# Optimization experiments

Hardware: AMD Instinct MI355X
Metric: run time of the kernel (lower is better)

## Reference

```python
import jax, jax.numpy as jnp
import numpy as np
from jax import lax

K_TOP = 4
NF1, NF2 = 6, 14
KS1, KS2 = 7, 5


def conv1d_grouped(x, w, b, groups, pad):
    # x: (B, Cin, L), w: (Cout, Cin//groups, K)
    y = lax.conv_general_dilated(x, w, window_strides=(1,), padding=[(pad, pad)],
                                 dimension_numbers=('NCH', 'OIH', 'NCH'),
                                 feature_group_count=groups)
    return y + b[None, :, None]


def kmax_pool(x, k):
    # order-preserving k-max along last axis
    idx = jnp.sort(lax.top_k(x, k)[1], axis=-1)
    return jnp.take_along_axis(x, idx, axis=-1)


def fold_sum(h, b, nf, rows, L):
    # h: (B, rows*nf, L) with group-major channel layout (rows groups of nf)
    h = h.reshape(b, rows, nf, L).transpose(0, 2, 1, 3)        # (B, nf, rows, L)
    h = h.reshape(b, nf, rows // 2, 2, L).sum(axis=3)          # Fold(2,2): sum adjacent row pairs
    return h.transpose(0, 2, 1, 3).reshape(b, (rows // 2) * nf, L)


def setup_inputs() -> dict:
    key = jax.random.key(0)
    ks = jax.random.split(key, 8)
    V, D, C, B, S = 50257, 256, 1000, 32, 1024
    x = jax.random.randint(ks[0], (B, S), 0, V)
    emb = jax.random.normal(ks[1], (V, D), jnp.float32)
    w1 = jax.random.normal(ks[2], (NF1 * D, 1, KS1), jnp.float32) * 0.1
    b1 = jnp.zeros((NF1 * D,), jnp.float32)
    w2 = jax.random.normal(ks[3], (NF2 * (D // 2), NF1, KS2), jnp.float32) * 0.05
    b2 = jnp.zeros((NF2 * (D // 2),), jnp.float32)
    wf = jax.random.normal(ks[4], (C, NF2 * (D // 4) * K_TOP), jnp.float32) * 0.02
    bf = jnp.zeros((C,), jnp.float32)
    return {"x": x, "emb": emb, "w1": w1, "b1": b1, "w2": w2, "b2": b2, "wf": wf, "bf": bf}


def reference(x, emb, w1, b1, w2, b2, wf, bf):
    D = emb.shape[1]
    B = x.shape[0]
    h = emb[x].transpose(0, 2, 1)                 # (B, D, S)
    h = conv1d_grouped(h, w1, b1, groups=D, pad=KS1 - 1)   # (B, 6D, S+6)
    L1 = h.shape[-1]
    h = fold_sum(h, B, NF1, D, L1)                # (B, 3D, L1)
    # dynamic k-max: layer 1 of 2 -> k = max(k_top, ceil(L/2))
    k1 = max(K_TOP, -(-L1 // 2))
    h = jnp.tanh(kmax_pool(h, k1))
    h = conv1d_grouped(h, w2, b2, groups=D // 2, pad=KS2 - 1)  # (B, 7D, k1+4)
    L2 = h.shape[-1]
    h = fold_sum(h, B, NF2, D // 2, L2)           # (B, 14*(D/4), L2)
    h = jnp.tanh(kmax_pool(h, K_TOP))             # (B, 14*(D/4), k_top)
    # dropout is identity in eval mode
    h = h.reshape(B, -1)
    return h @ wf.T + bf
```

## Files before the change

### kernel.cpp

```cpp
#include <hip/hip_runtime.h>
#include <hip/hip_bf16.h>


typedef __attribute__((ext_vector_type(8))) short short8;
typedef __attribute__((ext_vector_type(4))) float f32x4;
typedef __attribute__((ext_vector_type(2))) float f32x2;
typedef __attribute__((ext_vector_type(4))) int int4v;

union VPack { int4v i; short8 s; };

__device__ __forceinline__ float fast_tanh(float x) {
    float e = __expf(2.f * x);
    return 1.f - 2.f / (e + 1.f);
}

__device__ __forceinline__ unsigned fkey(float f) {
    unsigned u = __float_as_uint(f);
    return (u & 0x80000000u) ? ~u : (u | 0x80000000u);
}

__device__ __forceinline__ float fkey_inv(unsigned k) {
    unsigned u = (k & 0x80000000u) ? (k ^ 0x80000000u) : ~k;
    return __uint_as_float(u);
}

__device__ __forceinline__ unsigned f2bf_rne(float f) {
    unsigned u = __float_as_uint(f);
    return (u + 0x7fffu + ((u >> 16) & 1u)) >> 16;
}

__device__ __forceinline__ int prefix_cnt(unsigned long long m) {
    return (int)__builtin_amdgcn_mbcnt_hi((unsigned)(m >> 32),
                 __builtin_amdgcn_mbcnt_lo((unsigned)m, 0u));
}

__global__ __launch_bounds__(896) void stage12_kernel(
    const int* __restrict__ x, const float* __restrict__ emb,
    const float* __restrict__ w1, const float* __restrict__ b1,
    const float* __restrict__ w2, const float* __restrict__ b2,
    __hip_bfloat16* __restrict__ H)
{
    __shared__ __align__(16) float X[7448];
    __shared__ __align__(16) unsigned F[12 * 536];
    const int hw = blockIdx.x;
    const int logical = ((hw & 7) << 8) | (hw >> 3);
    const int b = logical >> 6;
    const int r2 = logical & 63;
    const int tid = threadIdx.x;
    const int w = tid >> 6;
    const int lane = tid & 63;
    float* e = X;

    const int half = (w >= 6) ? 1 : 0;
    const int c0 = __builtin_amdgcn_readfirstlane(
        (2 * (2 * r2 + half)) * 6 + ((w < 12) ? (w - half * 6) : 0));
    const int c1 = c0 + 6;
    float wA[7], wB[7];
#pragma unroll
    for (int t = 0; t < 7; ++t) { wA[t] = w1[c0 * 7 + t]; wB[t] = w1[c1 * 7 + t]; }
    const float bias = b1[c0] + b1[c1];
    const int bidx2 = __builtin_amdgcn_readfirstlane((2 * r2) * 14 + w);
    const float bias2 = b2[bidx2] + b2[bidx2 + 14];

    {
        const int l0 = tid - 6;
        const int l1 = tid + 890;
        int t0 = -1, t1 = -1;
        if (l0 >= 0 && l0 < 1024) t0 = x[(b << 10) + l0];
        if (tid < 208 && l1 < 1024) t1 = x[(b << 10) + l1];
        float4 v0 = {0.f, 0.f, 0.f, 0.f}, v1 = {0.f, 0.f, 0.f, 0.f};
        if (t0 >= 0) v0 = *(const float4*)(emb + ((size_t)t0 << 8) + (r2 << 2));
        if (t1 >= 0) v1 = *(const float4*)(emb + ((size_t)t1 << 8) + (r2 << 2));
        for (int i = tid; i < 12 * 536; i += 896) F[i] = 0u;
        e[0 * 1104 + tid] = v0.x; e[1 * 1104 + tid] = v0.y;
        e[2 * 1104 + tid] = v0.z; e[3 * 1104 + tid] = v0.w;
        if (tid < 208) {
            const int idx = tid + 896;
            e[0 * 1104 + idx] = v1.x; e[1 * 1104 + idx] = v1.y;
            e[2 * 1104 + idx] = v1.z; e[3 * 1104 + idx] = v1.w;
        }
    }
    __syncthreads();

    if (w < 12) {
        const float* ep0 = e + (2 * half) * 1104;
        const float* ep1 = ep0 + 1104;
        f32x2 wv[7];
#pragma unroll
        for (int t = 0; t < 7; ++t) wv[t] = f32x2{wA[t], wB[t]};

        const int pos0 = lane * 17;
        f32x2 win[7];
#pragma unroll
        for (int t = 0; t < 7; ++t) win[t] = f32x2{ep0[pos0 + t], ep1[pos0 + t]};

        unsigned key[17];
#pragma unroll
        for (int j = 0; j < 17; ++j) {
            f32x2 acc = f32x2{bias, 0.f};
#pragma unroll
            for (int t = 0; t < 7; ++t) acc += win[t] * wv[t];
            float a = acc.x + acc.y;
            key[j] = (pos0 + j < 1030) ? fkey(a) : 0u;
            if (j < 16) {
#pragma unroll
                for (int t = 0; t < 6; ++t) win[t] = win[t + 1];
                win[6] = f32x2{ep0[pos0 + j + 7], ep1[pos0 + j + 7]};
            }
        }

        unsigned T = 0u;
        for (int bit = 31; bit >= 0; --bit) {
            unsigned cand = T | (1u << bit);
            int cnt = 0;
#pragma unroll
            for (int j = 0; j < 17; ++j) cnt += (int)__popcll(__ballot(key[j] >= cand));
            if (cnt >= 515) T = cand;
            if (cnt == 515) break;
        }

        int gt_tot = 0, gt_run = 0, eq_run = 0;
#pragma unroll
        for (int j = 0; j < 17; ++j) {
            unsigned long long bg = __ballot(key[j] > T);
            unsigned long long be = __ballot(key[j] == T);
            gt_tot += (int)__popcll(bg);
            gt_run += prefix_cnt(bg);
            eq_run += prefix_cnt(be);
        }
        const int q = 515 - gt_tot;
        unsigned* Frow = F + w * 536;
#pragma unroll
        for (int j = 0; j < 17; ++j) {
            bool isgt = key[j] > T;
            bool iseq = key[j] == T;
            int pos = gt_run + (eq_run < q ? eq_run : q);
            if (isgt || (iseq && eq_run < q)) Frow[4 + pos] = key[j];
            gt_run += isgt ? 1 : 0;
            eq_run += iseq ? 1 : 0;
        }

#pragma unroll
        for (int it = 0; it < 9; ++it) {
            int i = 4 + lane + (it << 6);
            if (i < 519) {
                unsigned k = Frow[i];
                float v = fast_tanh(fkey_inv(k));
                unsigned h = f2bf_rne(v);
                float fh = __uint_as_float(h << 16);
                unsigned l = f2bf_rne(v - fh);
                Frow[i] = (k == 0u) ? 0u : ((h << 16) | l);
            }
        }
    }

    const int jA = lane & 15;
    const int q3 = lane >> 4;
    short8 Ah0, Ah1, Al0, Al1;
    {
        float wt[16];
#pragma unroll
        for (int mm = 0; mm < 16; ++mm) {
            float v = 0.f;
            if (mm < 15 && jA < 14) {
                const int irow = 3 * q3 + mm / 5;
                const int t = mm % 5;
                const int h2 = (irow >= 6) ? 1 : 0;
                v = w2[(((2 * r2 + h2) * 14 + jA) * 6 + (irow - 6 * h2)) * 5 + t];
            }
            wt[mm] = v;
        }
#pragma unroll
        for (int m = 0; m < 8; ++m) {
            unsigned h0 = f2bf_rne(wt[m]);
            float fh0 = __uint_as_float(h0 << 16);
            Ah0[m] = (short)h0;
            Al0[m] = (short)f2bf_rne(wt[m] - fh0);
            unsigned h1 = f2bf_rne(wt[8 + m]);
            float fh1 = __uint_as_float(h1 << 16);
            Ah1[m] = (short)h1;
            Al1[m] = (short)f2bf_rne(wt[8 + m] - fh1);
        }
    }
    __syncthreads();

    float* OUT = X;
    for (int tile = w; tile < 33; tile += 14) {
        const int p0 = tile << 4;
        const int bidx = (3 * q3) * 536 + p0 + jA;
        unsigned u[16];
#pragma unroll
        for (int mm = 0; mm < 15; ++mm) u[mm] = F[bidx + (mm / 5) * 536 + (mm % 5)];
        u[15] = 0u;
        VPack bh0, bl0, bh1, bl1;
#pragma unroll
        for (int k = 0; k < 4; ++k) {
            unsigned a = u[2 * k], bq = u[2 * k + 1];
            bh0.i[k] = (int)((a >> 16) | (bq & 0xffff0000u));
            bl0.i[k] = (int)((a & 0xffffu) | (bq << 16));
            unsigned c = u[8 + 2 * k], d = u[9 + 2 * k];
            bh1.i[k] = (int)((c >> 16) | (d & 0xffff0000u));
            bl1.i[k] = (int)((c & 0xffffu) | (d << 16));
        }
        f32x4 d0 = {0.f, 0.f, 0.f, 0.f};
        f32x4 d1 = {0.f, 0.f, 0.f, 0.f};
        d0 = __builtin_amdgcn_mfma_f32_16x16x32_bf16(Ah0, bh0.s, d0, 0, 0, 0);
        d1 = __builtin_amdgcn_mfma_f32_16x16x32_bf16(Ah1, bh1.s, d1, 0, 0, 0);
        d0 = __builtin_amdgcn_mfma_f32_16x16x32_bf16(Ah0, bl0.s, d0, 0, 0, 0);
        d1 = __builtin_amdgcn_mfma_f32_16x16x32_bf16(Ah1, bl1.s, d1, 0, 0, 0);
        d0 = __builtin_amdgcn_mfma_f32_16x16x32_bf16(Al0, bh0.s, d0, 0, 0, 0);
        d1 = __builtin_amdgcn_mfma_f32_16x16x32_bf16(Al1, bh1.s, d1, 0, 0, 0);
        float* orow = OUT + (q3 * 4) * 532 + p0 + jA;
#pragma unroll
        for (int r = 0; r < 4; ++r)
            if (q3 * 4 + r < 14) orow[r * 532] = d0[r] + d1[r];
    }
    __syncthreads();

    {
        const int j = w;
        const int base = lane * 9;
        float vv[9];
#pragma unroll
        for (int jj = 0; jj < 9; ++jj)
            vv[jj] = (base + jj < 519) ? OUT[j * 532 + base + jj] : -INFINITY;
        float sv[4]; int si[4];
#pragma unroll
        for (int it = 0; it < 4; ++it) {
            float m = vv[0]; int mi = base;
#pragma unroll
            for (int jj = 1; jj < 9; ++jj) { if (vv[jj] > m) { m = vv[jj]; mi = base + jj; } }
#pragma unroll
            for (int d = 1; d < 64; d <<= 1) {
                float om = __shfl_xor(m, d, 64);
                int omi = __shfl_xor(mi, d, 64);
                if (om > m || (om == m && omi < mi)) { m = om; mi = omi; }
            }
            sv[it] = m; si[it] = mi;
            int lj = mi - base;
#pragma unroll
            for (int jj = 0; jj < 9; ++jj) if (jj == lj) vv[jj] = -INFINITY;
        }
#define CSWAP(a, bq) { if (si[a] > si[bq]) { int ti = si[a]; si[a] = si[bq]; si[bq] = ti; \
                                             float tv = sv[a]; sv[a] = sv[bq]; sv[bq] = tv; } }
        CSWAP(0, 1) CSWAP(2, 3) CSWAP(0, 2) CSWAP(1, 3) CSWAP(1, 2)
#undef CSWAP
        if (lane == 0) {
            __hip_bfloat16* op = H + (size_t)b * 3584 + (r2 * 14 + j) * 4;
#pragma unroll
            for (int k = 0; k < 4; ++k) op[k] = __float2bfloat16(fast_tanh(sv[k] + bias2));
        }
    }
}

__global__ __launch_bounds__(512) void stage3_kernel(
    const __hip_bfloat16* __restrict__ Hb, const float* __restrict__ wf,
    const float* __restrict__ bfv, float* __restrict__ out)
{
    __shared__ __align__(16) float sred[8 * 256];
    const int nt = blockIdx.x % 63;
    const int mh = blockIdx.x / 63;
    const int w = threadIdx.x >> 6, lane = threadIdx.x & 63;
    const int row = lane & 15, quad = lane >> 4;
    const int c = nt * 16 + row;
    const bool cvalid = (c < 1000);
    const int kofs = w * 448 + quad * 8;
    const __hip_bfloat16* ap = Hb + (size_t)(mh * 16 + row) * 3584 + kofs;
    const float* bp = wf + (size_t)(cvalid ? c : 0) * 3584 + kofs;

    f32x4 acc = {0.f, 0.f, 0.f, 0.f};
#pragma unroll
    for (int it = 0; it < 14; ++it) {
        short8 a0 = *(const short8*)(ap + it * 32);
        float4 p0 = *(const float4*)(bp + it * 32);
        float4 p1 = *(const float4*)(bp + it * 32 + 4);
        short8 bfr;
        bfr[0] = (short)f2bf_rne(p0.x); bfr[1] = (short)f2bf_rne(p0.y);
        bfr[2] = (short)f2bf_rne(p0.z); bfr[3] = (short)f2bf_rne(p0.w);
        bfr[4] = (short)f2bf_rne(p1.x); bfr[5] = (short)f2bf_rne(p1.y);
        bfr[6] = (short)f2bf_rne(p1.z); bfr[7] = (short)f2bf_rne(p1.w);
        if (!cvalid) bfr = short8{0, 0, 0, 0, 0, 0, 0, 0};
        acc = __builtin_amdgcn_mfma_f32_16x16x32_bf16(a0, bfr, acc, 0, 0, 0);
    }
#pragma unroll
    for (int r_ = 0; r_ < 4; ++r_) sred[w * 256 + lane * 4 + r_] = acc[r_];
    __syncthreads();
    if (threadIdx.x < 64) {
        const int l2 = threadIdx.x;
        const int rr = l2 & 15, qq = l2 >> 4;
        const int cc = nt * 16 + rr;
        if (cc < 1000) {
            const float bias = bfv[cc];
#pragma unroll
            for (int r_ = 0; r_ < 4; ++r_) {
                float s = 0.f;
#pragma unroll
                for (int ww = 0; ww < 8; ++ww) s += sred[ww * 256 + l2 * 4 + r_];
                int brow = mh * 16 + qq * 4 + r_;
                out[brow * 1000 + cc] = s + bias;
            }
        }
    }
}

extern "C" void kernel_launch(void* const* d_in, const int* in_sizes, int n_in,
                              void* d_out, int out_size, void* d_ws, size_t ws_size,
                              hipStream_t stream) {
    const int* x      = (const int*)d_in[0];
    const float* emb  = (const float*)d_in[1];
    const float* w1   = (const float*)d_in[2];
    const float* b1   = (const float*)d_in[3];
    const float* w2   = (const float*)d_in[4];
    const float* b2   = (const float*)d_in[5];
    const float* wf   = (const float*)d_in[6];
    const float* bfv  = (const float*)d_in[7];

    __hip_bfloat16* H = (__hip_bfloat16*)d_ws;

    stage12_kernel<<<32 * 64, 896, 0, stream>>>(x, emb, w1, b1, w2, b2, H);
    stage3_kernel<<<126, 512, 0, stream>>>(H, wf, bfv, (float*)d_out);
}
```

Before: 238.1 us.

## Split final GEMM over K with atomics and reuse weight tile across both batch halves

The final linear layer now splits the K dimension into 4 chunks across blocks. Each block processes both 16-row batch tiles, so every converted wf fragment is reused for two MFMAs instead of being loaded twice by separate blocks. Partial sums are combined with atomicAdd into an output that a new kernel pre-fills with the bias. This halves the wf traffic and bf16 conversions, at the cost of an extra launch and atomics. It also makes the fp32 summation order nondeterministic.

```diff
diff --git a/kernel.cpp b/kernel.cpp
--- a/kernel.cpp
+++ b/kernel.cpp
@@ -253,25 +253,35 @@
     }
 }
 
-__global__ __launch_bounds__(512) void stage3_kernel(
-    const __hip_bfloat16* __restrict__ Hb, const float* __restrict__ wf,
+__global__ __launch_bounds__(256) void bias_init_kernel(
     const float* __restrict__ bfv, float* __restrict__ out)
 {
-    __shared__ __align__(16) float sred[8 * 256];
+    int idx = blockIdx.x * 256 + threadIdx.x;
+    if (idx < 32000) out[idx] = bfv[idx - (idx / 1000) * 1000];
+}
+
+__global__ __launch_bounds__(256) void stage3_kernel(
+    const __hip_bfloat16* __restrict__ Hb, const float* __restrict__ wf,
+    float* __restrict__ out)
+{
+    __shared__ __align__(16) float sred[2 * 4 * 256];
     const int nt = blockIdx.x % 63;
-    const int mh = blockIdx.x / 63;
+    const int kc = blockIdx.x / 63;
     const int w = threadIdx.x >> 6, lane = threadIdx.x & 63;
     const int row = lane & 15, quad = lane >> 4;
     const int c = nt * 16 + row;
     const bool cvalid = (c < 1000);
-    const int kofs = w * 448 + quad * 8;
-    const __hip_bfloat16* ap = Hb + (size_t)(mh * 16 + row) * 3584 + kofs;
+    const int kofs = kc * 896 + w * 224 + quad * 8;
+    const __hip_bfloat16* ap0 = Hb + (size_t)row * 3584 + kofs;
+    const __hip_bfloat16* ap1 = ap0 + (size_t)16 * 3584;
     const float* bp = wf + (size_t)(cvalid ? c : 0) * 3584 + kofs;
 
-    f32x4 acc = {0.f, 0.f, 0.f, 0.f};
-#pragma unroll
-    for (int it = 0; it < 14; ++it) {
-        short8 a0 = *(const short8*)(ap + it * 32);
+    f32x4 acc0 = {0.f, 0.f, 0.f, 0.f};
+    f32x4 acc1 = {0.f, 0.f, 0.f, 0.f};
+#pragma unroll
+    for (int it = 0; it < 7; ++it) {
+        short8 a0 = *(const short8*)(ap0 + it * 32);
+        short8 a1 = *(const short8*)(ap1 + it * 32);
         float4 p0 = *(const float4*)(bp + it * 32);
         float4 p1 = *(const float4*)(bp + it * 32 + 4);
         short8 bfr;
@@ -280,24 +290,28 @@
         bfr[4] = (short)f2bf_rne(p1.x); bfr[5] = (short)f2bf_rne(p1.y);
         bfr[6] = (short)f2bf_rne(p1.z); bfr[7] = (short)f2bf_rne(p1.w);
         if (!cvalid) bfr = short8{0, 0, 0, 0, 0, 0, 0, 0};
-        acc = __builtin_amdgcn_mfma_f32_16x16x32_bf16(a0, bfr, acc, 0, 0, 0);
-    }
-#pragma unroll
-    for (int r_ = 0; r_ < 4; ++r_) sred[w * 256 + lane * 4 + r_] = acc[r_];
+        acc0 = __builtin_amdgcn_mfma_f32_16x16x32_bf16(a0, bfr, acc0, 0, 0, 0);
+        acc1 = __builtin_amdgcn_mfma_f32_16x16x32_bf16(a1, bfr, acc1, 0, 0, 0);
+    }
+#pragma unroll
+    for (int r_ = 0; r_ < 4; ++r_) {
+        sred[(0 * 4 + w) * 256 + lane * 4 + r_] = acc0[r_];
+        sred[(1 * 4 + w) * 256 + lane * 4 + r_] = acc1[r_];
+    }
     __syncthreads();
-    if (threadIdx.x < 64) {
-        const int l2 = threadIdx.x;
+    if (threadIdx.x < 128) {
+        const int mt = threadIdx.x >> 6;
+        const int l2 = threadIdx.x & 63;
         const int rr = l2 & 15, qq = l2 >> 4;
         const int cc = nt * 16 + rr;
         if (cc < 1000) {
-            const float bias = bfv[cc];
+            const float* sp = sred + mt * 4 * 256;
 #pragma unroll
             for (int r_ = 0; r_ < 4; ++r_) {
-                float s = 0.f;
-#pragma unroll
-                for (int ww = 0; ww < 8; ++ww) s += sred[ww * 256 + l2 * 4 + r_];
-                int brow = mh * 16 + qq * 4 + r_;
-                out[brow * 1000 + cc] = s + bias;
+                float s = sp[0 * 256 + l2 * 4 + r_] + sp[1 * 256 + l2 * 4 + r_]
+                        + sp[2 * 256 + l2 * 4 + r_] + sp[3 * 256 + l2 * 4 + r_];
+                int brow = mt * 16 + qq * 4 + r_;
+                atomicAdd(&out[brow * 1000 + cc], s);
             }
         }
     }
@@ -317,6 +331,7 @@
 
     __hip_bfloat16* H = (__hip_bfloat16*)d_ws;
 
+    bias_init_kernel<<<125, 256, 0, stream>>>(bfv, (float*)d_out);
     stage12_kernel<<<32 * 64, 896, 0, stream>>>(x, emb, w1, b1, w2, b2, H);
-    stage3_kernel<<<126, 512, 0, stream>>>(H, wf, bfv, (float*)d_out);
-}
+    stage3_kernel<<<63 * 4, 256, 0, stream>>>(H, wf, (float*)d_out);
+}
```

Measured after the change: 235.9 us. No clear change (-0.9%).
